# Kernel tuning notes

Measured on AMD Instinct MI355X. Metric: run time of the kernel, lower is better.

## Reference

```python
import jax, jax.numpy as jnp
import numpy as np

NUM_Q = 2048
N = 512
D = 256
H = 8
LW = 25
B = 32
NUM_ATTN = 6  # base, local, skill_group, global, cross_base_local, cross_skill_global


def _layernorm(x, g, b, eps=1e-5):
    m = jnp.mean(x, axis=-1, keepdims=True)
    v = jnp.mean((x - m) ** 2, axis=-1, keepdims=True)
    return (x - m) / jnp.sqrt(v + eps) * g + b


def _mha(q, k, v, in_w, in_b, out_w, out_b, mask=None):
    # torch nn.MultiheadAttention math, batch-first layout. mask: bool, True = masked.
    Bq, Lq, d = q.shape
    Lk = k.shape[1]
    hd = d // H
    qh = (q @ in_w[:d].T + in_b[:d]).reshape(Bq, Lq, H, hd).transpose(0, 2, 1, 3)
    kh = (k @ in_w[d:2 * d].T + in_b[d:2 * d]).reshape(Bq, Lk, H, hd).transpose(0, 2, 1, 3)
    vh = (v @ in_w[2 * d:].T + in_b[2 * d:]).reshape(Bq, Lk, H, hd).transpose(0, 2, 1, 3)
    s = jnp.einsum('bhqd,bhkd->bhqk', qh, kh) / jnp.sqrt(jnp.asarray(hd, q.dtype))
    if mask is not None:
        s = jnp.where(mask, jnp.asarray(-1e9, s.dtype), s)
    w = jax.nn.softmax(s, axis=-1)
    o = jnp.einsum('bhqk,bhkd->bhqd', w, vh).transpose(0, 2, 1, 3).reshape(Bq, Lq, d)
    return o @ out_w.T + out_b, jnp.mean(w, axis=1)  # avg heads like torch default


def setup_inputs() -> dict:
    key = jax.random.key(0)
    ks = jax.random.split(key, 24)
    s = 0.02
    inp = {
        'q': jax.random.randint(ks[0], (B, N), 0, NUM_Q),
        'r': jax.random.randint(ks[1], (B, N), 0, 2),
        'qry': jax.random.randint(ks[2], (B, N), 0, NUM_Q),
        'M_emb': jax.random.normal(ks[3], (NUM_Q * 2, D), jnp.float32) * s,
        'E_emb': jax.random.normal(ks[4], (NUM_Q, D), jnp.float32) * s,
        'P': jax.random.normal(ks[5], (N, D), jnp.float32) * s,
        'attn_in_w': jax.random.normal(ks[6], (NUM_ATTN, 3 * D, D), jnp.float32) * s,
        'attn_in_b': jnp.zeros((NUM_ATTN, 3 * D), jnp.float32),
        'attn_out_w': jax.random.normal(ks[7], (NUM_ATTN, D, D), jnp.float32) * s,
        'attn_out_b': jnp.zeros((NUM_ATTN, D), jnp.float32),
        'skill_cluster_weights': jax.random.normal(ks[8], (NUM_Q, NUM_Q), jnp.float32) * s,
        'skill_proj_w': jax.random.normal(ks[9], (D, NUM_Q), jnp.float32) * s,
        'skill_proj_b': jnp.zeros((D,), jnp.float32),
        'skill_to_embed_w': jax.random.normal(ks[10], (D, N), jnp.float32) * s,
        'skill_to_embed_b': jnp.zeros((D,), jnp.float32),
        'ffn_w1': jax.random.normal(ks[11], (D, D), jnp.float32) * s,
        'ffn_b1': jnp.zeros((D,), jnp.float32),
        'ffn_w2': jax.random.normal(ks[12], (D, D), jnp.float32) * s,
        'ffn_b2': jnp.zeros((D,), jnp.float32),
        'ln1_g': jnp.ones((D,), jnp.float32),
        'ln1_b': jnp.zeros((D,), jnp.float32),
        'ln2_g': jnp.ones((D,), jnp.float32),
        'ln2_b': jnp.zeros((D,), jnp.float32),
        'pred_w': jax.random.normal(ks[13], (1, D), jnp.float32) * s,
        'pred_b': jnp.zeros((1,), jnp.float32),
    }
    return inp


def reference(q, r, qry, M_emb, E_emb, P, attn_in_w, attn_in_b, attn_out_w, attn_out_b,
              skill_cluster_weights, skill_proj_w, skill_proj_b, skill_to_embed_w,
              skill_to_embed_b, ffn_w1, ffn_b1, ffn_w2, ffn_b2, ln1_g, ln1_b, ln2_g,
              ln2_b, pred_w, pred_b):
    bsz = q.shape[0]
    x = q + NUM_Q * r                      # [B, N]
    M = M_emb[x] + P[None]                 # [B, N, D]
    E = E_emb[qry]                         # [B, N, D]
    causal = jnp.triu(jnp.ones((N, N), bool), 1)

    S_base, attn_weights_base = _mha(E, M, M, attn_in_w[0], attn_in_b[0],
                                     attn_out_w[0], attn_out_b[0], causal)
    S_base = _layernorm(S_base + M + E, ln1_g, ln1_b)

    # local windowed causal attention over last LW steps, zeros elsewhere
    loc = S_base[:, -LW:, :]
    local_causal = jnp.triu(jnp.ones((LW, LW), bool), 1)
    S_local, _ = _mha(loc, loc, loc, attn_in_w[1], attn_in_b[1],
                      attn_out_w[1], attn_out_b[1], local_causal)
    S_local = jnp.concatenate(
        [jnp.zeros((bsz, N - LW, D), S_base.dtype), S_local], axis=1)

    # skill-group: one_hot(q) @ softmax(W) == row gather (same math, no dense one-hot)
    sw = jax.nn.softmax(skill_cluster_weights, axis=-1)
    skill_group_repr = sw[q]                                  # [B, N, NUM_Q]
    skill_group_repr = skill_group_repr @ skill_proj_w.T + skill_proj_b  # [B, N, D]
    S_sg = jnp.einsum('bnd,bmd->bnm', S_base, skill_group_repr)          # [B, N, N]
    S_sg = S_sg @ skill_to_embed_w.T + skill_to_embed_b                  # [B, N, D]
    S_sg, _ = _mha(S_sg, S_sg, S_sg, attn_in_w[2], attn_in_b[2],
                   attn_out_w[2], attn_out_b[2])

    S_glob, _ = _mha(S_base, S_base, S_base, attn_in_w[3], attn_in_b[3],
                     attn_out_w[3], attn_out_b[3], causal)

    S_bl, _ = _mha(S_base, S_local, S_local, attn_in_w[4], attn_in_b[4],
                   attn_out_w[4], attn_out_b[4])
    S_sgl, _ = _mha(S_sg, S_glob, S_glob, attn_in_w[5], attn_in_b[5],
                    attn_out_w[5], attn_out_b[5])

    S = S_base + S_local + S_sg + S_glob + S_bl + S_sgl
    F = jax.nn.relu(S @ ffn_w1.T + ffn_b1) @ ffn_w2.T + ffn_b2
    F = _layernorm(F + S, ln2_g, ln2_b)
    p = jax.nn.sigmoid(F @ pred_w.T + pred_b).squeeze(-1)     # [B, N]
    return p, attn_weights_base
```

## Files before the change

### kernel.cpp

```cpp
#include <hip/hip_runtime.h>
#include <hip/hip_bf16.h>

#define B_  32
#define N_  512
#define D_  256
#define H_  8
#define HD_ 32
#define LW_ 25

typedef __hip_bfloat16 bf;
typedef __attribute__((ext_vector_type(8))) short short8;
typedef __attribute__((ext_vector_type(4))) float f32x4;

__device__ __forceinline__ void gload16(const void* g, void* l) {
    __builtin_amdgcn_global_load_lds(
        (const __attribute__((address_space(1))) unsigned int*)g,
        (__attribute__((address_space(3))) unsigned int*)l, 16, 0, 0);
}

#define QSC 0.2550349f

__global__ __launch_bounds__(256) void gemm2_k(
    const bf* Aq, const bf* Akv, const bf* W, const float* bias,
    float* Cf, bf* Cb, float* Cacc,
// ... 29 lines not shown

    const int sidx0 = tid, sidx1 = tid + 256;
    long long arow0, arow1;
    {
        int m = m0 + (sidx0 >> 2);
        arow0 = (long long)(m / rowsPerA) * aBatch + (long long)(m % rowsPerA) * aRstride;
        m = m0 + (sidx1 >> 2);
        arow1 = (long long)(m / rowsPerA) * aBatch + (long long)(m % rowsPerA) * aRstride;
    }
    const long long wrow0 = (long long)(o0 + (sidx0 >> 2)) * K;
    const long long wrow1 = (long long)(o0 + (sidx1 >> 2)) * K;
    const int ac0 = (sidx0 & 3) * 8, ac1 = (sidx1 & 3) * 8;

    f32x4 acc[4][4];
    #pragma unroll
    for (int mt = 0; mt < 4; mt++)
        #pragma unroll
        for (int nt = 0; nt < 4; nt++)
            acc[mt][nt] = (f32x4)0.f;

    for (int k0 = kStart; k0 < kEnd; k0 += 32) {
        const long long ka = (long long)k0 * aKMul;
        gload16(A + arow0 + ka + ac0, As + sidx0 * 8);
        gload16(A + arow1 + ka + ac1, As + sidx1 * 8);
        gload16(Wp + wrow0 + k0 + ac0, Bs + sidx0 * 8);
        gload16(Wp + wrow1 + k0 + ac1, Bs + sidx1 * 8);
        __syncthreads();
        short8 af[4], bfr[4];
        #pragma unroll
        for (int mt = 0; mt < 4; mt++)
            af[mt] = *(const short8*)(As + (wm + mt * 16 + col) * 32 + quad * 8);
        #pragma unroll
        for (int nt = 0; nt < 4; nt++)
            bfr[nt] = *(const short8*)(Bs + (wn + nt * 16 + col) * 32 + quad * 8);
        #pragma unroll
        for (int mt = 0; mt < 4; mt++)
            #pragma unroll
            for (int nt = 0; nt < 4; nt++)
                acc[mt][nt] = __builtin_amdgcn_mfma_f32_16x16x32_bf16(
                    af[mt], bfr[nt], acc[mt][nt], 0, 0, 0);
        __syncthreads();
    }

    #pragma unroll
    for (int mt = 0; mt < 4; mt++) {
        #pragma unroll
        for (int nt = 0; nt < 4; nt++) {
            const int o = o0 + wn + nt * 16 + col;
            #pragma unroll
            for (int r = 0; r < 4; r++) {
                const int m = m0 + wm + mt * 16 + quad * 4 + r;
                if (m >= M) continue;
                float v = acc[mt][nt][r];
                if (bias) v += bias[o];
                if (flags & 1) v = fmaxf(v, 0.f);
                if (flags & 4) {
                    atomicAdd(Cf + (long long)m * Onum + o, v);
                } else {
                    long long ci = (long long)m * Onum + o;
                    if (flags & 2) v += Cf[ci];
                    if (Cf) Cf[ci] = v;
                    if (Cb) Cb[ci] = __float2bfloat16(v);
                    if (Cacc) Cacc[ci] += v;
                }
            }
        }
    }
}

__global__ __launch_bounds__(256) void gemm64_k(
    const bf* A, const bf* W, const float* bias,
    float* Cf, bf* Cb, float* Cacc,
    int M, int K, int Onum,
    int rowsPerA, long long aBatch, int aRstride, long long aKMul,
    long long aZ, long long wZ, long long cZ, int flags)
{
    __shared__ __align__(16) bf As[64 * 32];
    __shared__ __align__(16) bf Bs[64 * 32];
    const int tid = threadIdx.x;
    const int o0 = blockIdx.x * 64;
    const int m0 = blockIdx.y * 64;
    const int z  = blockIdx.z;
    A += (long long)z * aZ;
    W += (long long)z * wZ;
    if (Cf)   Cf   += (long long)z * cZ;
    if (Cb)   Cb   += (long long)z * cZ;
    if (Cacc) Cacc += (long long)z * cZ;

    const int w = tid >> 6, lane = tid & 63;
    const int col = lane & 15, quad = lane >> 4;
    const int wm = (w & 1) * 32;
    const int wn = (w >> 1) * 32;

    const int srow = tid >> 2;
    const int sac  = (tid & 3) * 8;
    long long arow;
    {
        const int m = m0 + srow;
        arow = (long long)(m / rowsPerA) * aBatch
             + (long long)(m % rowsPerA) * aRstride;
    }
    const long long wrow = (long long)(o0 + srow) * K;

    f32x4 acc[2][2];
    acc[0][0] = (f32x4)0.f; acc[0][1] = (f32x4)0.f;
    acc[1][0] = (f32x4)0.f; acc[1][1] = (f32x4)0.f;

    for (int k0 = 0; k0 < K; k0 += 32) {
        gload16(A + arow + (long long)k0 * aKMul + sac, As + tid * 8);
        gload16(W + wrow + k0 + sac, Bs + tid * 8);
        __syncthreads();
        short8 af[2], bfr[2];
        #pragma unroll
        for (int mt = 0; mt < 2; mt++)
            af[mt] = *(const short8*)(As + (wm + mt * 16 + col) * 32 + quad * 8);
        #pragma unroll
        for (int nt = 0; nt < 2; nt++)
            bfr[nt] = *(const short8*)(Bs + (wn + nt * 16 + col) * 32 + quad * 8);
        #pragma unroll
        for (int mt = 0; mt < 2; mt++)
            #pragma unroll
            for (int nt = 0; nt < 2; nt++)
                acc[mt][nt] = __builtin_amdgcn_mfma_f32_16x16x32_bf16(
                    af[mt], bfr[nt], acc[mt][nt], 0, 0, 0);
        __syncthreads();
    }

    #pragma unroll
    for (int mt = 0; mt < 2; mt++) {
        #pragma unroll
        for (int nt = 0; nt < 2; nt++) {
            const int o = o0 + wn + nt * 16 + col;
            #pragma unroll
            for (int r = 0; r < 4; r++) {
                const int m = m0 + wm + mt * 16 + quad * 4 + r;
                if (m >= M) continue;
                float v = acc[mt][nt][r];
                if (bias) v += bias[o];
                if (flags & 1) v = fmaxf(v, 0.f);
                if (flags & 4) {
                    atomicAdd(Cf + (long long)m * Onum + o, v);
                } else {
                    long long ci = (long long)m * Onum + o;
                    if (flags & 2) v += Cf[ci];
                    if (Cf) Cf[ci] = v;
                    if (Cb) Cb[ci] = __float2bfloat16(v);
                    if (Cacc) Cacc[ci] += v;
                }
            }
        }
    }
}

template<int LP2>
__global__ __launch_bounds__(256) void dgemm_k(
    const bf* Aq, const bf* Akv, const bf* W, const float* bias,
    int M, int K,
    int rowsPerA, long long aBatch, int aRstride, long long aKMul,
    bf* Qd, bf* Kd, bf* Vd, int Lseq, int Lvt)
{
    const int tid = threadIdx.x;
    const int w = tid >> 6, lane = tid & 63;
    const int col = lane & 15, quad = lane >> 4;
    const int nmb = gridDim.x / 12;
    int ob, mb;
    if ((nmb & 7) == 0) {
        const int xcd = blockIdx.x & 7;
        const int q = blockIdx.x >> 3;
        mb = xcd + 8 * (q / 12);
        ob = q % 12;
    } else {
        ob = blockIdx.x % 12;
        mb = blockIdx.x / 12;
    }
    const int o0 = ob * 64;
    const int m0 = mb * 128;
    const bf* A = (o0 >= 256) ? Akv : Aq;
    const bf* Wp = W;

    const long long aStep = 32 * aKMul;
    const bf* aP[2];
    #pragma unroll
    for (int mt = 0; mt < 2; mt++) {
        const int m = m0 + w * 32 + mt * 16 + col;
        aP[mt] = A + (long long)(m / rowsPerA) * aBatch
               + (long long)(m % rowsPerA) * aRstride + quad * 8;
    }
    const bf* wP[4];
    #pragma unroll
    for (int ot = 0; ot < 4; ot++)
        wP[ot] = Wp + (long long)(o0 + ot * 16 + col) * K + quad * 8;

    f32x4 acc[2][4];
    #pragma unroll
    for (int mt = 0; mt < 2; mt++)
        #pragma unroll
        for (int ot = 0; ot < 4; ot++)
            acc[mt][ot] = (f32x4)0.f;

    short8 af0 = *(const short8*)aP[0];
    short8 af1 = *(const short8*)aP[1];
    short8 bw[4];
    #pragma unroll
    for (int ot = 0; ot < 4; ot++) bw[ot] = *(const short8*)wP[ot];
    aP[0] += aStep; aP[1] += aStep;
    #pragma unroll
    for (int ot = 0; ot < 4; ot++) wP[ot] += 32;

    const int kc1 = K >> 5;
    for (int kc = 0; kc < kc1 - 1; kc++) {
        short8 naf0 = *(const short8*)aP[0];
        short8 naf1 = *(const short8*)aP[1];
        short8 nbw[4];
        #pragma unroll
        for (int ot = 0; ot < 4; ot++) nbw[ot] = *(const short8*)wP[ot];
        aP[0] += aStep; aP[1] += aStep;
        #pragma unroll
        for (int ot = 0; ot < 4; ot++) wP[ot] += 32;

        #pragma unroll
        for (int ot = 0; ot < 4; ot++) {
            acc[0][ot] = __builtin_amdgcn_mfma_f32_16x16x32_bf16(
                af0, bw[ot], acc[0][ot], 0, 0, 0);
            acc[1][ot] = __builtin_amdgcn_mfma_f32_16x16x32_bf16(
                af1, bw[ot], acc[1][ot], 0, 0, 0);
        }
        af0 = naf0; af1 = naf1;
        #pragma unroll
        for (int ot = 0; ot < 4; ot++) bw[ot] = nbw[ot];
    }
    #pragma unroll
    for (int ot = 0; ot < 4; ot++) {
        acc[0][ot] = __builtin_amdgcn_mfma_f32_16x16x32_bf16(
            af0, bw[ot], acc[0][ot], 0, 0, 0);
        acc[1][ot] = __builtin_amdgcn_mfma_f32_16x16x32_bf16(
            af1, bw[ot], acc[1][ot], 0, 0, 0);
    }

    const int which = o0 >> 8;
    #pragma unroll
    for (int mt = 0; mt < 2; mt++) {
        const int mb4 = m0 + w * 32 + mt * 16 + quad * 4;
        #pragma unroll
        for (int ot = 0; ot < 4; ot++) {
            const int o  = o0 + ot * 16 + col;
            const int j2 = o & 31;
            const int hh = (o >> 5) & 7;
            if (LP2 > 0) {
                const int bb  = mb4 >> LP2;
                const int nn0 = mb4 & ((1 << LP2) - 1);
                const int bh  = bb * H_ + hh;
                float v0 = acc[mt][ot][0], v1 = acc[mt][ot][1],
                      v2 = acc[mt][ot][2], v3 = acc[mt][ot][3];
                if (bias) {
                    const float bv = bias[o];
                    v0 += bv; v1 += bv; v2 += bv; v3 += bv;
                }
                if (which == 0) {
                    bf* q = Qd + ((size_t)bh * Lseq + nn0) * HD_ + j2;
                    q[0]      = __float2bfloat16(v0 * QSC);
                    q[HD_]    = __float2bfloat16(v1 * QSC);
                    q[2*HD_]  = __float2bfloat16(v2 * QSC);
                    q[3*HD_]  = __float2bfloat16(v3 * QSC);
                } else if (which == 1) {
                    bf* kd = Kd + ((size_t)bh * Lseq + nn0) * HD_ + j2;
                    kd[0]     = __float2bfloat16(v0);
                    kd[HD_]   = __float2bfloat16(v1);
                    kd[2*HD_] = __float2bfloat16(v2);
                    kd[3*HD_] = __float2bfloat16(v3);
                } else {
                    __align__(8) bf pk[4];
                    pk[0] = __float2bfloat16(v0);
                    pk[1] = __float2bfloat16(v1);
                    pk[2] = __float2bfloat16(v2);
                    pk[3] = __float2bfloat16(v3);
                    *(ushort4*)(Vd + ((size_t)bh * HD_ + j2) * Lvt + nn0) =
                        *(const ushort4*)pk;
                }
            } else {
                #pragma unroll
                for (int r = 0; r < 4; r++) {
                    const int m = mb4 + r;
                    if (m >= M) continue;
                    float v = acc[mt][ot][r];
                    if (bias) v += bias[o];
                    const int bb = m / Lseq, nn = m % Lseq;
                    const int bh = bb * H_ + hh;
                    if (which == 0) {
                        Qd[((size_t)bh * Lseq + nn) * HD_ + j2] =
                            __float2bfloat16(v * QSC);
                    } else if (which == 1) {
                        Kd[((size_t)bh * Lseq + nn) * HD_ + j2] = __float2bfloat16(v);
                    } else {
                        Vd[((size_t)bh * HD_ + j2) * Lvt + nn] = __float2bfloat16(v);
                    }
                }
            }
        }
    }
}

template<int CAUSAL, int STATS>
__global__ __launch_bounds__(256) void fattn_k(
    const bf* __restrict__ Qb, const bf* __restrict__ Kb,
    const bf* __restrict__ Vtb, bf* __restrict__ O,
    float2* __restrict__ St, int L, int Lvt)
{
    __shared__ __align__(16) bf Sh[4][16][40];
    const int tid = threadIdx.x;
    const int w = tid >> 6, lane = tid & 63;
    const int col = lane & 15, quad = lane >> 4;
    const int bh = blockIdx.x;
    const int yt = CAUSAL ? (int)(gridDim.y - 1 - blockIdx.y) : (int)blockIdx.y;
    const int q0 = yt * 64 + w * 16;
    const int NCH = L >> 5;
    const int cmax = CAUSAL ? min(NCH - 1, (q0 + 15) >> 5) : (NCH - 1);

    const bf* Qh = Qb  + (size_t)bh * L * HD_;
    const bf* Kh = Kb  + (size_t)bh * L * HD_;
    const bf* Vh = Vtb + (size_t)bh * HD_ * Lvt;

    const short8 aq = *(const short8*)(Qh + (size_t)(q0 + col) * HD_ + quad * 8);

    float m[4]   = {-3e38f, -3e38f, -3e38f, -3e38f};
    float sdp[4] = {0.f, 0.f, 0.f, 0.f};
    f32x4 oacc[2];
    oacc[0] = (f32x4)0.f; oacc[1] = (f32x4)0.f;

    const int qrow = q0 + quad * 4;

    auto process = [&](short8 kf0, short8 kf1, short8 vf0, short8 vf1,
                       int c, bool domask) {
        f32x4 s0 = __builtin_amdgcn_mfma_f32_16x16x32_bf16(
            aq, kf0, (f32x4)0.f, 0, 0, 0);
        f32x4 s1 = __builtin_amdgcn_mfma_f32_16x16x32_bf16(
            aq, kf1, (f32x4)0.f, 0, 0, 0);
        if (domask) {
            const int key0 = c * 32 + col;
            #pragma unroll
            for (int r = 0; r < 4; r++) {
                if (key0 > qrow + r)      s0[r] = -1e9f;
                if (key0 + 16 > qrow + r) s1[r] = -1e9f;
            }
        }
        float pml[4];
        #pragma unroll
        for (int r = 0; r < 4; r++)
            pml[r] = fmaxf(s0[r], s1[r]);
        const int okr = (pml[0] <= m[0] + 8.f) && (pml[1] <= m[1] + 8.f)
                     && (pml[2] <= m[2] + 8.f) && (pml[3] <= m[3] + 8.f);
        if (!__all(okr)) {
            #pragma unroll
            for (int r = 0; r < 4; r++) {
                float pm = pml[r];
                #pragma unroll
                for (int off = 1; off < 16; off <<= 1)
                    pm = fmaxf(pm, __shfl_xor(pm, off));
                const float mn = fmaxf(m[r], pm);
                const float scl = __builtin_amdgcn_exp2f(m[r] - mn);
                m[r] = mn;
                sdp[r] *= scl;
                oacc[0][r] *= scl;
                oacc[1][r] *= scl;
            }
        }
        #pragma unroll
        for (int r = 0; r < 4; r++) {
            float e0 = __builtin_amdgcn_exp2f(s0[r] - m[r]);
            float e1 = __builtin_amdgcn_exp2f(s1[r] - m[r]);
            sdp[r] += e0 + e1;
            Sh[w][quad * 4 + r][col]      = __float2bfloat16(e0);
            Sh[w][quad * 4 + r][16 + col] = __float2bfloat16(e1);
        }
        const short8 ap = *(const short8*)(&Sh[w][col][quad * 8]);
        oacc[0] = __builtin_amdgcn_mfma_f32_16x16x32_bf16(ap, vf0, oacc[0], 0, 0, 0);
        oacc[1] = __builtin_amdgcn_mfma_f32_16x16x32_bf16(ap, vf1, oacc[1], 0, 0, 0);
    };

    const bf* kP = Kh + (size_t)col * HD_ + quad * 8;
    const bf* vP = Vh + (size_t)col * Lvt + quad * 8;
    const int kHf = 16 * HD_;
    const int vHf = 16 * Lvt;

    short8 kf0 = *(const short8*)kP;
    short8 kf1 = *(const short8*)(kP + kHf);
    short8 vf0 = *(const short8*)vP;
    short8 vf1 = *(const short8*)(vP + vHf);
    kP += 32 * HD_; vP += 32;

    for (int c = 0; c < cmax; c++) {
        short8 nk0 = *(const short8*)kP;
        short8 nk1 = *(const short8*)(kP + kHf);
        short8 nv0 = *(const short8*)vP;
        short8 nv1 = *(const short8*)(vP + vHf);
        kP += 32 * HD_; vP += 32;
        process(kf0, kf1, vf0, vf1, c, false);
        kf0 = nk0; kf1 = nk1; vf0 = nv0; vf1 = nv1;
    }
    process(kf0, kf1, vf0, vf1, cmax, CAUSAL != 0);

    float inv[4];
    #pragma unroll
    for (int r = 0; r < 4; r++) {
        #pragma unroll
        for (int off = 1; off < 16; off <<= 1)
            sdp[r] += __shfl_xor(sdp[r], off);
        inv[r] = 1.f / sdp[r];
    }
    if (STATS && col == 0) {
        #pragma unroll
        for (int r = 0; r < 4; r++)
            St[(size_t)bh * L + q0 + quad * 4 + r] = make_float2(m[r], inv[r]);
    }
    #pragma unroll
    for (int hf = 0; hf < 2; hf++)
        #pragma unroll
        for (int r = 0; r < 4; r++)
            O[((size_t)bh * L + q0 + quad * 4 + r) * HD_ + hf * 16 + col] =
                __float2bfloat16(oacc[hf][r] * inv[r]);
}

__global__ __launch_bounds__(256) void meanp_k(
    const bf* __restrict__ Qb, const bf* __restrict__ Kb,
    const float2* __restrict__ St, float* __restrict__ meanW)
{
    const int tid = threadIdx.x;
    const int w = tid >> 6, lane = tid & 63;
    const int col = lane & 15, quad = lane >> 4;
    const int b = blockIdx.x;
    const int q0 = blockIdx.y * 16;
    const int cmax = (q0 + 15) >> 5;

    f32x4 mreg[4][2];
    #pragma unroll
    for (int cc = 0; cc < 4; cc++)
        #pragma unroll
        for (int hf = 0; hf < 2; hf++) mreg[cc][hf] = (f32x4)0.f;

    for (int h = 0; h < H_; h++) {
        const int bh = b * H_ + h;
        const bf* Qh = Qb + (size_t)bh * N_ * HD_;
        const bf* Kh = Kb + (size_t)bh * N_ * HD_;
        const short8 aq = *(const short8*)(Qh + (size_t)(q0 + col) * HD_ + quad * 8);
        float mrow[4], irow[4];
        #pragma unroll
        for (int r = 0; r < 4; r++) {
            float2 s2 = St[(size_t)bh * N_ + q0 + quad * 4 + r];
            mrow[r] = s2.x; irow[r] = s2.y;
        }
        #pragma unroll
        for (int cc = 0; cc < 4; cc++) {
            const int c = w + 4 * cc;
            if (c > cmax) continue;
            #pragma unroll
            for (int hf = 0; hf < 2; hf++) {
                const int key = c * 32 + hf * 16 + col;
                const short8 kf = *(const short8*)(Kh + (size_t)key * HD_ + quad * 8);
                f32x4 sc = __builtin_amdgcn_mfma_f32_16x16x32_bf16(
                    aq, kf, (f32x4)0.f, 0, 0, 0);
                #pragma unroll
                for (int r = 0; r < 4; r++) {
                    float p = (key > q0 + quad * 4 + r) ? 0.f
                        : __builtin_amdgcn_exp2f(sc[r] - mrow[r]) * irow[r];
                    mreg[cc][hf][r] += p;
                }
            }
        }
    }

    const size_t base = ((size_t)b * N_ + q0) * N_;
    #pragma unroll
    for (int cc = 0; cc < 4; cc++) {
        const int c = w + 4 * cc;
        #pragma unroll
        for (int hf = 0; hf < 2; hf++)
            #pragma unroll
            for (int r = 0; r < 4; r++)
                meanW[base + (size_t)(quad * 4 + r) * N_ + c * 32 + hf * 16 + col]
                    = mreg[cc][hf][r] * 0.125f;
    }
}

#define SP 520
#define OPS 34

template<int MEAN, int QT>
__global__ __launch_bounds__(256) void attn5_k(
    const bf* Qb, const bf* Kb, const bf* Vtb,
    bf* O, float* meanW, int L, int Lvt, int causal, int nhl)
{
    __shared__ __align__(16) bf Sh[16 * SP];
    __shared__ __align__(16) float redm[2][16][4];
    __shared__ __align__(16) float invRow[16];
    __shared__ __align__(16) float Opart[4][16][OPS];
    const int tid = threadIdx.x;
    const int w = tid >> 6, lane = tid & 63;
    const int col = lane & 15, quad = lane >> 4;
    const int q0 = blockIdx.y * (16 * QT);
    const int bh0 = blockIdx.x * nhl;
    const int NCH = (L + 31) >> 5;
    const int qLast = q0 + (QT - 1) * 16;
    const int cmaxP = causal ? min(NCH - 1, (qLast + 15) >> 5) : (NCH - 1);
    const int nccP = (w <= cmaxP) ? ((cmaxP - w) >> 2) + 1 : 0;

    f32x4 mreg[4][2];
    if (MEAN) {
        #pragma unroll
        for (int cc = 0; cc < 4; cc++)
            #pragma unroll
            for (int hf = 0; hf < 2; hf++) mreg[cc][hf] = (f32x4)0.f;
    }

    for (int hh = 0; hh < nhl; hh++) {
        const int bh = bh0 + hh;
        const bf* Qh = Qb  + (size_t)bh * L * HD_;
        const bf* Kh = Kb  + (size_t)bh * L * HD_;
        const bf* Vh = Vtb + (size_t)bh * HD_ * Lvt;

        short8 aq[QT];
        #pragma unroll
        for (int t = 0; t < QT; t++) {
            aq[t] = (short8)(short)0;
            const int n = q0 + t * 16 + col;
            if (n < L)
                aq[t] = *(const short8*)(Qh + (size_t)n * HD_ + quad * 8);
        }
        short8 kfr[4][2], vfr[4][2];
        #pragma unroll
        for (int cc = 0; cc < 4; cc++) {
            if (cc >= nccP) break;
            const int c = w + 4 * cc;
            #pragma unroll
            for (int hf = 0; hf < 2; hf++) {
                const int key = c * 32 + hf * 16 + col;
                kfr[cc][hf] = (short8)(short)0;
                if (key < L)
                    kfr[cc][hf] = *(const short8*)(Kh + (size_t)key * HD_ + quad * 8);
                vfr[cc][hf] = *(const short8*)(Vh + (size_t)(hf * 16 + col) * Lvt
                                                + c * 32 + quad * 8);
            }
        }

        #pragma unroll
        for (int t = 0; t < QT; t++) {
            const int qt0 = q0 + t * 16;
            const int cmaxT = causal ? min(NCH - 1, (qt0 + 15) >> 5) : (NCH - 1);
            const int nccT = (w <= cmaxT) ? ((cmaxT - w) >> 2) + 1 : 0;

            f32x4 sc[4][2];
            #pragma unroll
            for (int cc = 0; cc < 4; cc++) {
                if (cc >= nccT) break;
// ... 107 lines not shown
            for (int e = tid; e < 512; e += 256) {
                int row = e >> 5, d = e & 31;
                float v = (Opart[0][row][d] + Opart[1][row][d] +
                           Opart[2][row][d] + Opart[3][row][d]) * invRow[row];
                int n = qt0 + row;
                if (n < L)
                    O[((size_t)bh * L + n) * HD_ + d] = __float2bfloat16(v);
            }
            if (t + 1 < QT || hh + 1 < nhl) __syncthreads();
        }
    }

    if (MEAN) {
        const size_t base = ((size_t)blockIdx.x * N_ + q0) * N_;
        #pragma unroll
        for (int cc = 0; cc < 4; cc++) {
            const int c = w + 4 * cc;
            #pragma unroll
            for (int hf = 0; hf < 2; hf++)
                #pragma unroll
                for (int r = 0; r < 4; r++)
                    meanW[base + (size_t)(quad * 4 + r) * N_ + c * 32 + hf * 16 + col]
                        = mreg[cc][hf][r] * 0.125f;
        }
    }
}

__global__ void conv_k(const float* s, bf* d, int n) {
    int i = blockIdx.x * 256 + threadIdx.x;
    if (i < n) d[i] = __float2bfloat16(s[i]);
}

__global__ __launch_bounds__(256) void rowsoftmax_k(const float* in, bf* out) {
    __shared__ float red[256];
    const long long row = blockIdx.x;
    const int t = threadIdx.x;
    const float* ip = in + row * 2048;
    bf* op = out + row * 2048;
    float m = -3e38f;
    for (int k = t; k < 2048; k += 256) m = fmaxf(m, ip[k]);
    red[t] = m; __syncthreads();
    for (int s = 128; s > 0; s >>= 1) { if (t < s) red[t] = fmaxf(red[t], red[t + s]); __syncthreads(); }
    m = red[0]; __syncthreads();
    float ps = 0.f;
    float ev[8];
    #pragma unroll
    for (int i = 0; i < 8; i++) { ev[i] = __expf(ip[t + i * 256] - m); ps += ev[i]; }
    red[t] = ps; __syncthreads();
    for (int s = 128; s > 0; s >>= 1) { if (t < s) red[t] += red[t + s]; __syncthreads(); }
    const float inv = 1.f / red[0];
    #pragma unroll
    for (int i = 0; i < 8; i++) op[t + i * 256] = __float2bfloat16(ev[i] * inv);
}

__global__ void embed_k(const int* q, const int* r, const int* qry,
                        const float* Memb, const float* Eemb, const float* P,
                        float* M, float* E, bf* Mh, bf* Eh) {
    const int i = blockIdx.x; const int t = threadIdx.x;
    const int n = i & (N_ - 1);
    const int x = q[i] + 2048 * r[i];
    float mv = Memb[(long long)x * D_ + t] + P[(long long)n * D_ + t];
    float evv = Eemb[(long long)qry[i] * D_ + t];
    M[(long long)i * D_ + t] = mv;  Mh[(long long)i * D_ + t] = __float2bfloat16(mv);
    E[(long long)i * D_ + t] = evv; Eh[(long long)i * D_ + t] = __float2bfloat16(evv);
}

__global__ void gather_k(const int* q, const float* T, const float* spb, bf* G) {
    const int i = blockIdx.x; const int t = threadIdx.x;
    G[(long long)i * D_ + t] = __float2bfloat16(T[(long long)q[i] * D_ + t] + spb[t]);
}

__global__ __launch_bounds__(256) void ln_k(const float* xa, const float* xb, const float* xc,
                                            const float* g, const float* bta,
                                            float* outF, bf* outB, float* out2) {
    __shared__ float red[256];
    const long long row = blockIdx.x;
    const int t = threadIdx.x;
    float v = xa[row * D_ + t];
    if (xb) v += xb[row * D_ + t];
    if (xc) v += xc[row * D_ + t];
    red[t] = v; __syncthreads();
    for (int s = 128; s > 0; s >>= 1) { if (t < s) red[t] += red[t + s]; __syncthreads(); }
    const float mean = red[0] * (1.f / 256.f);
    __syncthreads();
    const float d = v - mean;
    red[t] = d * d; __syncthreads();
    for (int s = 128; s > 0; s >>= 1) { if (t < s) red[t] += red[t + s]; __syncthreads(); }
    const float var = red[0] * (1.f / 256.f);
    const float y = d * rsqrtf(var + 1e-5f) * g[t] + bta[t];
    if (outF) outF[row * D_ + t] = y;
    if (outB) outB[row * D_ + t] = __float2bfloat16(y);
    if (out2) out2[row * D_ + t] = y;
}

__global__ void scatterlocal_k(const float* tail, bf* Slocalh, float* Sacc) {
    const int i = blockIdx.x; const int t = threadIdx.x;
    const int n = i & (N_ - 1), b = i >> 9;
    float v = 0.f;
    if (n >= N_ - LW_) {
        v = tail[((long long)(b * LW_ + (n - (N_ - LW_)))) * D_ + t];
        Sacc[(long long)i * D_ + t] += v;
    }
    Slocalh[(long long)i * D_ + t] = __float2bfloat16(v);
}

__global__ void zero4_k(float4* p) {
    p[(long long)blockIdx.x * 256 + threadIdx.x] = make_float4(0.f, 0.f, 0.f, 0.f);
}

__global__ __launch_bounds__(256) void pred_k(const float* F, const float* pw, const float* pb,
                                              float* out) {
    const int tid = threadIdx.x;
    const int wave = tid >> 6, lane = tid & 63;
    const long long row = (long long)blockIdx.x * 4 + wave;
    const float* fp = F + row * D_ + lane * 4;
    float s = 0.f;
    #pragma unroll
    for (int j = 0; j < 4; j++) s += fp[j] * pw[lane * 4 + j];
    #pragma unroll
    for (int off = 32; off > 0; off >>= 1) s += __shfl_down(s, off);
    if (lane == 0) {
        float p = 1.f / (1.f + __expf(-(s + pb[0])));
        out[row] = p;
    }
}

static void gemm2(hipStream_t st, const bf* Aq, const bf* Akv,
                  const bf* W, const float* bias, float* Cf, bf* Cb, float* Cacc,
                  int M, int K, int Onum,
                  int rowsPerA, long long aBatch, int aRstride, long long aKMul,
                  long long aZ, long long wZ, long long cZ, int Z,
                  int qkv, int flags, int splitKc,
                  bf* Qd, bf* Kd, bf* Vd, int Lseq, int Lvt)
{
    dim3 g(Onum / 128, (M + 127) / 128, Z), blk(256, 1, 1);
    gemm2_k<<<g, blk, 0, st>>>(Aq, Akv, W, bias, Cf, Cb, Cacc, M, K, Onum,
                               rowsPerA, aBatch, aRstride, aKMul,
                               aZ, wZ, cZ, qkv, flags, splitKc,
                               Qd, Kd, Vd, Lseq, Lvt);
}

static void gemm64(hipStream_t st, const bf* A, const bf* W, const float* bias,
                   float* Cf, bf* Cb, float* Cacc, int M, int K, int Onum,
                   int rowsPerA, long long aBatch, int aRstride, long long aKMul,
                   long long aZ, long long wZ, long long cZ, int Z, int flags)
{
    dim3 g(Onum / 64, (M + 63) / 64, Z), blk(256, 1, 1);
    gemm64_k<<<g, blk, 0, st>>>(A, W, bias, Cf, Cb, Cacc, M, K, Onum,
                                rowsPerA, aBatch, aRstride, aKMul,
                                aZ, wZ, cZ, flags);
}

static void dqkv(hipStream_t st, const bf* Aq, const bf* Akv,
                 const bf* W, const float* bias, int M, int K,
                 int rowsPerA, long long aBatch, int aRstride, long long aKMul,
                 bf* Qd, bf* Kd, bf* Vd, int Lseq, int Lvt)
{
    dim3 g(((M + 127) / 128) * 12, 1, 1), blk(256, 1, 1);
    if (Lseq == 512 && (M & 127) == 0)
        dgemm_k<9><<<g, blk, 0, st>>>(Aq, Akv, W, bias, M, K,
                                      rowsPerA, aBatch, aRstride, aKMul,
                                      Qd, Kd, Vd, Lseq, Lvt);
    else
        dgemm_k<0><<<g, blk, 0, st>>>(Aq, Akv, W, bias, M, K,
                                      rowsPerA, aBatch, aRstride, aKMul,
                                      Qd, Kd, Vd, Lseq, Lvt);
}

extern "C" void kernel_launch(void* const* d_in, const int* in_sizes, int n_in,
                              void* d_out, int out_size, void* d_ws, size_t ws_size,
                              hipStream_t stream)
{
    const int* qi  = (const int*)d_in[0];
    const int* ri  = (const int*)d_in[1];
    const int* qry = (const int*)d_in[2];
    const float* Memb = (const float*)d_in[3];
    const float* Eemb = (const float*)d_in[4];
    const float* Pp   = (const float*)d_in[5];
    const float* ainw = (const float*)d_in[6];
    const float* ainb = (const float*)d_in[7];
    const float* aoutw= (const float*)d_in[8];
    const float* aoutb= (const float*)d_in[9];
    const float* scw  = (const float*)d_in[10];
    const float* spw  = (const float*)d_in[11];
    const float* spb  = (const float*)d_in[12];
    const float* stew = (const float*)d_in[13];
    const float* steb = (const float*)d_in[14];
    const float* fw1  = (const float*)d_in[15];
    const float* fb1  = (const float*)d_in[16];
    const float* fw2  = (const float*)d_in[17];
    const float* fb2  = (const float*)d_in[18];
    const float* l1g  = (const float*)d_in[19];
    const float* l1b  = (const float*)d_in[20];
    const float* l2g  = (const float*)d_in[21];
    const float* l2b  = (const float*)d_in[22];
    const float* pw   = (const float*)d_in[23];
    const float* pb   = (const float*)d_in[24];
    float* out = (float*)d_out;
    float* outW = out + B_ * N_;

    const size_t BND = (size_t)B_ * N_ * D_;
    float* ws = (float*)d_ws;
    float* b10 = ws;
    float* b0  = ws + 1 * BND;
    float* b1  = ws + 2 * BND;
    float* b8  = ws + 3 * BND;
    float* b9  = ws + 4 * BND;
    float* hp  = ws + 5 * BND;
    bf* b0h  = (bf*)(hp + 0 * (BND / 2));
    bf* b1h  = (bf*)(hp + 1 * (BND / 2));
    bf* b2h  = (bf*)(hp + 2 * (BND / 2));
    bf* b7h  = (bf*)(hp + 3 * (BND / 2));
    bf* b8h  = (bf*)(hp + 4 * (BND / 2));
    bf* b9h  = (bf*)(hp + 5 * (BND / 2));
    bf* b10h = (bf*)(hp + 6 * (BND / 2));
    bf* b11h = (bf*)(hp + 7 * (BND / 2));
    bf* Qb   = (bf*)(hp + 8 * (BND / 2));
    bf* Kb   = (bf*)(hp + 9 * (BND / 2));
    bf* Vtb  = (bf*)(hp + 10 * (BND / 2));
    bf* Ob   = (bf*)(hp + 11 * (BND / 2));
    bf* BNNb = (bf*)(hp + 12 * (BND / 2));
    float* Ttab = hp + 12 * (BND / 2) + BND;
    bf* SWb  = (bf*)(Ttab + 2048 * 256);
    bf* Wb   = SWb + (size_t)2048 * 2048;
    bf* ainwB = Wb;
    bf* aoutwB = ainwB + 6 * 768 * 256;
    bf* spwB  = aoutwB + 6 * 256 * 256;
    bf* stewB = spwB + 256 * 2048;
    bf* fw1B  = stewB + 256 * 512;
    bf* fw2B  = fw1B + 256 * 256;
    const int BNrows = B_ * N_;
    const int BH = B_ * H_;
    const long long OBAT = 8LL * N_ * HD_;
    const long long OBATL = 8LL * LW_ * HD_;

    conv_k<<<(6*768*256 + 255)/256, 256, 0, stream>>>(ainw, ainwB, 6*768*256);
    conv_k<<<(6*256*256 + 255)/256, 256, 0, stream>>>(aoutw, aoutwB, 6*256*256);
    conv_k<<<(256*2048 + 255)/256, 256, 0, stream>>>(spw, spwB, 256*2048);
    conv_k<<<(256*512 + 255)/256, 256, 0, stream>>>(stew, stewB, 256*512);
    conv_k<<<(256*256 + 255)/256, 256, 0, stream>>>(fw1, fw1B, 256*256);
    conv_k<<<(256*256 + 255)/256, 256, 0, stream>>>(fw2, fw2B, 256*256);

    rowsoftmax_k<<<2048, 256, 0, stream>>>(scw, SWb);
    zero4_k<<<(2048 * 256) / 1024, 256, 0, stream>>>((float4*)Ttab);
    gemm2(stream, SWb, SWb, spwB, nullptr, Ttab, nullptr, nullptr, 2048, 2048, 256,
          2048, 0, 2048, 1, 0, 0, 0, 8, 0, 4, 256, nullptr, nullptr, nullptr, 0, 0);

    embed_k<<<BNrows, 256, 0, stream>>>(qi, ri, qry, Memb, Eemb, Pp, b0, b1, b0h, b1h);

    dqkv(stream, b1h, b0h, ainwB + 0, ainb + 0, BNrows, 256,
         BNrows, 0, 256, 1, Qb, Kb, Vtb, N_, N_);
    fattn_k<1, 1><<<dim3(BH, 8), 256, 0, stream>>>(Qb, Kb, Vtb, Ob, (float2*)b8, N_, N_);
    meanp_k<<<dim3(B_, 32), 256, 0, stream>>>(Qb, Kb, (const float2*)b8, outW);
    gemm64(stream, Ob, aoutwB + 0, aoutb + 0, b10, nullptr, nullptr, BNrows, 256, 256,
           N_, OBAT, HD_, N_, 0, 0, 0, 1, 0);
    ln_k<<<BNrows, 256, 0, stream>>>(b10, b0, b1, l1g, l1b, nullptr, b2h, b10);

    dqkv(stream, b2h + (size_t)(N_ - LW_) * D_, b2h + (size_t)(N_ - LW_) * D_,
         ainwB + 1 * 196608, ainb + 768, B_ * LW_, 256,
         LW_, (long long)N_ * D_, 256, 1, Qb, Kb, Vtb, LW_, 32);
    attn5_k<0, 2><<<dim3(BH, 1), 256, 0, stream>>>(Qb, Kb, Vtb, Ob, nullptr, LW_, 32, 1, 1);
    gemm64(stream, Ob, aoutwB + 1 * 65536, aoutb + 256, b0, nullptr, nullptr, B_ * LW_,
           256, 256, LW_, OBATL, HD_, LW_, 0, 0, 0, 1, 0);
    scatterlocal_k<<<BNrows, 256, 0, stream>>>(b0, b7h, b10);

    gather_k<<<BNrows, 256, 0, stream>>>(qi, Ttab, spb, b1h);
    gemm64(stream, b2h, b1h, nullptr, nullptr, BNNb, nullptr, N_, 256, N_,
           N_, 0, 256, 1, (long long)N_ * D_, (long long)N_ * D_, (long long)N_ * N_,
           B_, 0);
    gemm64(stream, BNNb, stewB, steb, nullptr, b11h, nullptr, BNrows, 512, 256,
           BNrows, 0, 512, 1, 0, 0, 0, 1, 0);
    dqkv(stream, b11h, b11h, ainwB + 2 * 196608, ainb + 2 * 768, BNrows, 256,
         BNrows, 0, 256, 1, Qb, Kb, Vtb, N_, N_);
    fattn_k<0, 0><<<dim3(BH, 8), 256, 0, stream>>>(Qb, Kb, Vtb, Ob, nullptr, N_, N_);
    gemm64(stream, Ob, aoutwB + 2 * 65536, aoutb + 2 * 256, b8, b8h, b10, BNrows,
           256, 256, N_, OBAT, HD_, N_, 0, 0, 0, 1, 0);

    dqkv(stream, b2h, b2h, ainwB + 3 * 196608, ainb + 3 * 768, BNrows, 256,
         BNrows, 0, 256, 1, Qb, Kb, Vtb, N_, N_);
    fattn_k<1, 0><<<dim3(BH, 8), 256, 0, stream>>>(Qb, Kb, Vtb, Ob, nullptr, N_, N_);
    gemm64(stream, Ob, aoutwB + 3 * 65536, aoutb + 3 * 256, b9, b9h, b10, BNrows,
           256, 256, N_, OBAT, HD_, N_, 0, 0, 0, 1, 0);

    dqkv(stream, b2h, b7h, ainwB + 4 * 196608, ainb + 4 * 768, BNrows, 256,
         BNrows, 0, 256, 1, Qb, Kb, Vtb, N_, N_);
    fattn_k<0, 0><<<dim3(BH, 8), 256, 0, stream>>>(Qb, Kb, Vtb, Ob, nullptr, N_, N_);
    gemm64(stream, Ob, aoutwB + 4 * 65536, aoutb + 4 * 256, b10, nullptr, nullptr, BNrows,
           256, 256, N_, OBAT, HD_, N_, 0, 0, 0, 1, 2);

    dqkv(stream, b8h, b9h, ainwB + 5 * 196608, ainb + 5 * 768, BNrows, 256,
         BNrows, 0, 256, 1, Qb, Kb, Vtb, N_, N_);
    fattn_k<0, 0><<<dim3(BH, 8), 256, 0, stream>>>(Qb, Kb, Vtb, Ob, nullptr, N_, N_);
    gemm64(stream, Ob, aoutwB + 5 * 65536, aoutb + 5 * 256, b10, b10h, nullptr, BNrows,
           256, 256, N_, OBAT, HD_, N_, 0, 0, 0, 1, 2);

    gemm64(stream, b10h, fw1B, fb1, nullptr, b11h, nullptr, BNrows, 256, 256,
           BNrows, 0, 256, 1, 0, 0, 0, 1, 1);
    gemm64(stream, b11h, fw2B, fb2, b0, nullptr, nullptr, BNrows, 256, 256,
           BNrows, 0, 256, 1, 0, 0, 0, 1, 0);
    ln_k<<<BNrows, 256, 0, stream>>>(b0, b10, nullptr, l2g, l2b, b1, nullptr, nullptr);
    pred_k<<<BNrows / 4, 256, 0, stream>>>(b1, pw, pb, out);
}
```

Measured before the change: 850.4 us.

## Software-pipeline flash attention PV with double-buffered P; fully unroll QKV GEMM K loop

The attention kernel now computes the P·V MFMA for the previous key chunk while the current chunk's QK scores and softmax are computed, using a double-buffered shared-memory P tile and a peeled first and last iteration. The first chunk initialises the running max directly instead of starting from a sentinel. The QKV projection GEMM makes K a template constant and fully unrolls the K loop, replacing the manual register prefetch. This hides MFMA and LDS latency at the cost of more registers and more complex control flow, which could reduce occupancy.

```diff
diff --git a/kernel.cpp b/kernel.cpp
--- a/kernel.cpp
+++ b/kernel.cpp
@@ -205,10 +205,10 @@
     }
 }
 
-template<int LP2>
+template<int LP2, int KC>
 __global__ __launch_bounds__(256) void dgemm_k(
     const bf* Aq, const bf* Akv, const bf* W, const float* bias,
-    int M, int K,
+    int M,
     int rowsPerA, long long aBatch, int aRstride, long long aKMul,
     bf* Qd, bf* Kd, bf* Vd, int Lseq, int Lvt)
 {
@@ -229,9 +229,8 @@
     const int o0 = ob * 64;
     const int m0 = mb * 128;
     const bf* A = (o0 >= 256) ? Akv : Aq;
-    const bf* Wp = W;
-
-    const long long aStep = 32 * aKMul;
+    const int K = KC * 32;
+
     const bf* aP[2];
     #pragma unroll
     for (int mt = 0; mt < 2; mt++) {
@@ -242,7 +241,7 @@
     const bf* wP[4];
     #pragma unroll
     for (int ot = 0; ot < 4; ot++)
-        wP[ot] = Wp + (long long)(o0 + ot * 16 + col) * K + quad * 8;
+        wP[ot] = W + (long long)(o0 + ot * 16 + col) * K + quad * 8;
 
     f32x4 acc[2][4];
     #pragma unroll
@@ -251,43 +250,19 @@
         for (int ot = 0; ot < 4; ot++)
             acc[mt][ot] = (f32x4)0.f;
 
-    short8 af0 = *(const short8*)aP[0];
-    short8 af1 = *(const short8*)aP[1];
-    short8 bw[4];
-    #pragma unroll
-    for (int ot = 0; ot < 4; ot++) bw[ot] = *(const short8*)wP[ot];
-    aP[0] += aStep; aP[1] += aStep;
-    #pragma unroll
-    for (int ot = 0; ot < 4; ot++) wP[ot] += 32;
-
-    const int kc1 = K >> 5;
-    for (int kc = 0; kc < kc1 - 1; kc++) {
-        short8 naf0 = *(const short8*)aP[0];
-        short8 naf1 = *(const short8*)aP[1];
-        short8 nbw[4];
-        #pragma unroll
-        for (int ot = 0; ot < 4; ot++) nbw[ot] = *(const short8*)wP[ot];
-        aP[0] += aStep; aP[1] += aStep;
-        #pragma unroll
-        for (int ot = 0; ot < 4; ot++) wP[ot] += 32;
-
+    #pragma unroll
+    for (int kc = 0; kc < KC; kc++) {
+        const long long ka = (long long)kc * 32 * aKMul;
+        const short8 af0 = *(const short8*)(aP[0] + ka);
+        const short8 af1 = *(const short8*)(aP[1] + ka);
         #pragma unroll
         for (int ot = 0; ot < 4; ot++) {
+            const short8 bfg = *(const short8*)(wP[ot] + kc * 32);
             acc[0][ot] = __builtin_amdgcn_mfma_f32_16x16x32_bf16(
-                af0, bw[ot], acc[0][ot], 0, 0, 0);
+                af0, bfg, acc[0][ot], 0, 0, 0);
             acc[1][ot] = __builtin_amdgcn_mfma_f32_16x16x32_bf16(
-                af1, bw[ot], acc[1][ot], 0, 0, 0);
-        }
-        af0 = naf0; af1 = naf1;
-        #pragma unroll
-        for (int ot = 0; ot < 4; ot++) bw[ot] = nbw[ot];
-    }
-    #pragma unroll
-    for (int ot = 0; ot < 4; ot++) {
-        acc[0][ot] = __builtin_amdgcn_mfma_f32_16x16x32_bf16(
-            af0, bw[ot], acc[0][ot], 0, 0, 0);
-        acc[1][ot] = __builtin_amdgcn_mfma_f32_16x16x32_bf16(
-            af1, bw[ot], acc[1][ot], 0, 0, 0);
+                af1, bfg, acc[1][ot], 0, 0, 0);
+        }
     }
 
     const int which = o0 >> 8;
@@ -359,7 +334,7 @@
     const bf* __restrict__ Vtb, bf* __restrict__ O,
     float2* __restrict__ St, int L, int Lvt)
 {
-    __shared__ __align__(16) bf Sh[4][16][40];
+    __shared__ __align__(16) bf Sh[4][2][16][40];
     const int tid = threadIdx.x;
     const int w = tid >> 6, lane = tid & 63;
     const int col = lane & 15, quad = lane >> 4;
@@ -375,27 +350,77 @@
 
     const short8 aq = *(const short8*)(Qh + (size_t)(q0 + col) * HD_ + quad * 8);
 
-    float m[4]   = {-3e38f, -3e38f, -3e38f, -3e38f};
+    float m[4];
     float sdp[4] = {0.f, 0.f, 0.f, 0.f};
     f32x4 oacc[2];
     oacc[0] = (f32x4)0.f; oacc[1] = (f32x4)0.f;
 
     const int qrow = q0 + quad * 4;
-
-    auto process = [&](short8 kf0, short8 kf1, short8 vf0, short8 vf1,
-                       int c, bool domask) {
+    const int kHf = 16 * HD_;
+    const int vHf = 16 * Lvt;
+
+    const bf* kP = Kh + (size_t)col * HD_ + quad * 8;
+    const bf* vP = Vh + (size_t)col * Lvt + quad * 8;
+
+    short8 kf0 = *(const short8*)kP;
+    short8 kf1 = *(const short8*)(kP + kHf);
+    short8 vp0 = *(const short8*)vP;
+    short8 vp1 = *(const short8*)(vP + vHf);
+    kP += 32 * HD_; vP += 32;
+    short8 kn0 = *(const short8*)kP;
+    short8 kn1 = *(const short8*)(kP + kHf);
+    short8 vn0 = *(const short8*)vP;
+    short8 vn1 = *(const short8*)(vP + vHf);
+    kP += 32 * HD_; vP += 32;
+
+    {
         f32x4 s0 = __builtin_amdgcn_mfma_f32_16x16x32_bf16(
             aq, kf0, (f32x4)0.f, 0, 0, 0);
         f32x4 s1 = __builtin_amdgcn_mfma_f32_16x16x32_bf16(
             aq, kf1, (f32x4)0.f, 0, 0, 0);
-        if (domask) {
-            const int key0 = c * 32 + col;
+        if (CAUSAL && cmax == 0) {
+            const int key0 = col;
             #pragma unroll
             for (int r = 0; r < 4; r++) {
                 if (key0 > qrow + r)      s0[r] = -1e9f;
                 if (key0 + 16 > qrow + r) s1[r] = -1e9f;
             }
         }
+        #pragma unroll
+        for (int r = 0; r < 4; r++) {
+            float pm = fmaxf(s0[r], s1[r]);
+            #pragma unroll
+            for (int off = 1; off < 16; off <<= 1)
+                pm = fmaxf(pm, __shfl_xor(pm, off));
+            m[r] = pm;
+            float e0 = __builtin_amdgcn_exp2f(s0[r] - pm);
+            float e1 = __builtin_amdgcn_exp2f(s1[r] - pm);
+            sdp[r] = e0 + e1;
+            Sh[w][0][quad * 4 + r][col]      = __float2bfloat16(e0);
+            Sh[w][0][quad * 4 + r][16 + col] = __float2bfloat16(e1);
+        }
+    }
+    kf0 = kn0; kf1 = kn1;
+    short8 vc0 = vn0, vc1 = vn1;
+
+    for (int c = 1; c < cmax; c++) {
+        kn0 = *(const short8*)kP;
+        kn1 = *(const short8*)(kP + kHf);
+        vn0 = *(const short8*)vP;
+        vn1 = *(const short8*)(vP + vHf);
+        kP += 32 * HD_; vP += 32;
+
+        f32x4 s0 = __builtin_amdgcn_mfma_f32_16x16x32_bf16(
+            aq, kf0, (f32x4)0.f, 0, 0, 0);
+        f32x4 s1 = __builtin_amdgcn_mfma_f32_16x16x32_bf16(
+            aq, kf1, (f32x4)0.f, 0, 0, 0);
+
+        {
+            const short8 ap = *(const short8*)(&Sh[w][(c - 1) & 1][col][quad * 8]);
+            oacc[0] = __builtin_amdgcn_mfma_f32_16x16x32_bf16(ap, vp0, oacc[0], 0, 0, 0);
+            oacc[1] = __builtin_amdgcn_mfma_f32_16x16x32_bf16(ap, vp1, oacc[1], 0, 0, 0);
+        }
+
         float pml[4];
         #pragma unroll
         for (int r = 0; r < 4; r++)
@@ -417,40 +442,76 @@
                 oacc[1][r] *= scl;
             }
         }
+
         #pragma unroll
         for (int r = 0; r < 4; r++) {
             float e0 = __builtin_amdgcn_exp2f(s0[r] - m[r]);
             float e1 = __builtin_amdgcn_exp2f(s1[r] - m[r]);
             sdp[r] += e0 + e1;
-            Sh[w][quad * 4 + r][col]      = __float2bfloat16(e0);
-            Sh[w][quad * 4 + r][16 + col] = __float2bfloat16(e1);
-        }
-        const short8 ap = *(const short8*)(&Sh[w][col][quad * 8]);
-        oacc[0] = __builtin_amdgcn_mfma_f32_16x16x32_bf16(ap, vf0, oacc[0], 0, 0, 0);
-        oacc[1] = __builtin_amdgcn_mfma_f32_16x16x32_bf16(ap, vf1, oacc[1], 0, 0, 0);
-    };
-
-    const bf* kP = Kh + (size_t)col * HD_ + quad * 8;
-    const bf* vP = Vh + (size_t)col * Lvt + quad * 8;
-    const int kHf = 16 * HD_;
-    const int vHf = 16 * Lvt;
-
-    short8 kf0 = *(const short8*)kP;
-    short8 kf1 = *(const short8*)(kP + kHf);
-    short8 vf0 = *(const short8*)vP;
-    short8 vf1 = *(const short8*)(vP + vHf);
-    kP += 32 * HD_; vP += 32;
-
-    for (int c = 0; c < cmax; c++) {
-        short8 nk0 = *(const short8*)kP;
-        short8 nk1 = *(const short8*)(kP + kHf);
-        short8 nv0 = *(const short8*)vP;
-        short8 nv1 = *(const short8*)(vP + vHf);
-        kP += 32 * HD_; vP += 32;
-        process(kf0, kf1, vf0, vf1, c, false);
-        kf0 = nk0; kf1 = nk1; vf0 = nv0; vf1 = nv1;
-    }
-    process(kf0, kf1, vf0, vf1, cmax, CAUSAL != 0);
+            Sh[w][c & 1][quad * 4 + r][col]      = __float2bfloat16(e0);
+            Sh[w][c & 1][quad * 4 + r][16 + col] = __float2bfloat16(e1);
+        }
+
+        vp0 = vc0; vp1 = vc1;
+        vc0 = vn0; vc1 = vn1;
+        kf0 = kn0; kf1 = kn1;
+    }
+
+    if (cmax >= 1) {
+        f32x4 s0 = __builtin_amdgcn_mfma_f32_16x16x32_bf16(
+            aq, kf0, (f32x4)0.f, 0, 0, 0);
+        f32x4 s1 = __builtin_amdgcn_mfma_f32_16x16x32_bf16(
+            aq, kf1, (f32x4)0.f, 0, 0, 0);
+        if (CAUSAL) {
+            const int key0 = cmax * 32 + col;
+            #pragma unroll
+            for (int r = 0; r < 4; r++) {
+                if (key0 > qrow + r)      s0[r] = -1e9f;
+                if (key0 + 16 > qrow + r) s1[r] = -1e9f;
+            }
+        }
+        {
+            const short8 ap = *(const short8*)(&Sh[w][(cmax - 1) & 1][col][quad * 8]);
+            oacc[0] = __builtin_amdgcn_mfma_f32_16x16x32_bf16(ap, vp0, oacc[0], 0, 0, 0);
+            oacc[1] = __builtin_amdgcn_mfma_f32_16x16x32_bf16(ap, vp1, oacc[1], 0, 0, 0);
+        }
+        float pml[4];
+        #pragma unroll
+        for (int r = 0; r < 4; r++)
+            pml[r] = fmaxf(s0[r], s1[r]);
+        const int okr = (pml[0] <= m[0] + 8.f) && (pml[1] <= m[1] + 8.f)
+                     && (pml[2] <= m[2] + 8.f) && (pml[3] <= m[3] + 8.f);
+        if (!__all(okr)) {
+            #pragma unroll
+            for (int r = 0; r < 4; r++) {
+                float pm = pml[r];
+                #pragma unroll
+                for (int off = 1; off < 16; off <<= 1)
+                    pm = fmaxf(pm, __shfl_xor(pm, off));
+                const float mn = fmaxf(m[r], pm);
+                const float scl = __builtin_amdgcn_exp2f(m[r] - mn);
+                m[r] = mn;
+                sdp[r] *= scl;
+                oacc[0][r] *= scl;
+                oacc[1][r] *= scl;
+            }
+        }
+        #pragma unroll
+        for (int r = 0; r < 4; r++) {
+            float e0 = __builtin_amdgcn_exp2f(s0[r] - m[r]);
+            float e1 = __builtin_amdgcn_exp2f(s1[r] - m[r]);
+            sdp[r] += e0 + e1;
+            Sh[w][cmax & 1][quad * 4 + r][col]      = __float2bfloat16(e0);
+            Sh[w][cmax & 1][quad * 4 + r][16 + col] = __float2bfloat16(e1);
+        }
+        vp0 = vc0; vp1 = vc1;
+    }
+
+    {
+        const short8 ap = *(const short8*)(&Sh[w][cmax & 1][col][quad * 8]);
+        oacc[0] = __builtin_amdgcn_mfma_f32_16x16x32_bf16(ap, vp0, oacc[0], 0, 0, 0);
+        oacc[1] = __builtin_amdgcn_mfma_f32_16x16x32_bf16(ap, vp1, oacc[1], 0, 0, 0);
+    }
 
     float inv[4];
     #pragma unroll
@@ -864,19 +925,19 @@
 }
 
 static void dqkv(hipStream_t st, const bf* Aq, const bf* Akv,
-                 const bf* W, const float* bias, int M, int K,
+                 const bf* W, const float* bias, int M,
                  int rowsPerA, long long aBatch, int aRstride, long long aKMul,
                  bf* Qd, bf* Kd, bf* Vd, int Lseq, int Lvt)
 {
     dim3 g(((M + 127) / 128) * 12, 1, 1), blk(256, 1, 1);
     if (Lseq == 512 && (M & 127) == 0)
-        dgemm_k<9><<<g, blk, 0, st>>>(Aq, Akv, W, bias, M, K,
-                                      rowsPerA, aBatch, aRstride, aKMul,
-                                      Qd, Kd, Vd, Lseq, Lvt);
+        dgemm_k<9, 8><<<g, blk, 0, st>>>(Aq, Akv, W, bias, M,
+                                         rowsPerA, aBatch, aRstride, aKMul,
+                                         Qd, Kd, Vd, Lseq, Lvt);
     else
-        dgemm_k<0><<<g, blk, 0, st>>>(Aq, Akv, W, bias, M, K,
-                                      rowsPerA, aBatch, aRstride, aKMul,
-                                      Qd, Kd, Vd, Lseq, Lvt);
+        dgemm_k<0, 8><<<g, blk, 0, st>>>(Aq, Akv, W, bias, M,
+                                         rowsPerA, aBatch, aRstride, aKMul,
+                                         Qd, Kd, Vd, Lseq, Lvt);
 }
 
 extern "C" void kernel_launch(void* const* d_in, const int* in_sizes, int n_in,
@@ -960,7 +1021,7 @@
 
     embed_k<<<BNrows, 256, 0, stream>>>(qi, ri, qry, Memb, Eemb, Pp, b0, b1, b0h, b1h);
 
-    dqkv(stream, b1h, b0h, ainwB + 0, ainb + 0, BNrows, 256,
+    dqkv(stream, b1h, b0h, ainwB + 0, ainb + 0, BNrows,
          BNrows, 0, 256, 1, Qb, Kb, Vtb, N_, N_);
     fattn_k<1, 1><<<dim3(BH, 8), 256, 0, stream>>>(Qb, Kb, Vtb, Ob, (float2*)b8, N_, N_);
     meanp_k<<<dim3(B_, 32), 256, 0, stream>>>(Qb, Kb, (const float2*)b8, outW);
@@ -969,7 +1030,7 @@
     ln_k<<<BNrows, 256, 0, stream>>>(b10, b0, b1, l1g, l1b, nullptr, b2h, b10);
 
     dqkv(stream, b2h + (size_t)(N_ - LW_) * D_, b2h + (size_t)(N_ - LW_) * D_,
-         ainwB + 1 * 196608, ainb + 768, B_ * LW_, 256,
+         ainwB + 1 * 196608, ainb + 768, B_ * LW_,
          LW_, (long long)N_ * D_, 256, 1, Qb, Kb, Vtb, LW_, 32);
     attn5_k<0, 2><<<dim3(BH, 1), 256, 0, stream>>>(Qb, Kb, Vtb, Ob, nullptr, LW_, 32, 1, 1);
     gemm64(stream, Ob, aoutwB + 1 * 65536, aoutb + 256, b0, nullptr, nullptr, B_ * LW_,
@@ -982,25 +1043,25 @@
            B_, 0);
     gemm64(stream, BNNb, stewB, steb, nullptr, b11h, nullptr, BNrows, 512, 256,
            BNrows, 0, 512, 1, 0, 0, 0, 1, 0);
-    dqkv(stream, b11h, b11h, ainwB + 2 * 196608, ainb + 2 * 768, BNrows, 256,
+    dqkv(stream, b11h, b11h, ainwB + 2 * 196608, ainb + 2 * 768, BNrows,
          BNrows, 0, 256, 1, Qb, Kb, Vtb, N_, N_);
     fattn_k<0, 0><<<dim3(BH, 8), 256, 0, stream>>>(Qb, Kb, Vtb, Ob, nullptr, N_, N_);
     gemm64(stream, Ob, aoutwB + 2 * 65536, aoutb + 2 * 256, b8, b8h, b10, BNrows,
            256, 256, N_, OBAT, HD_, N_, 0, 0, 0, 1, 0);
 
-    dqkv(stream, b2h, b2h, ainwB + 3 * 196608, ainb + 3 * 768, BNrows, 256,
+    dqkv(stream, b2h, b2h, ainwB + 3 * 196608, ainb + 3 * 768, BNrows,
          BNrows, 0, 256, 1, Qb, Kb, Vtb, N_, N_);
     fattn_k<1, 0><<<dim3(BH, 8), 256, 0, stream>>>(Qb, Kb, Vtb, Ob, nullptr, N_, N_);
     gemm64(stream, Ob, aoutwB + 3 * 65536, aoutb + 3 * 256, b9, b9h, b10, BNrows,
            256, 256, N_, OBAT, HD_, N_, 0, 0, 0, 1, 0);
 
-    dqkv(stream, b2h, b7h, ainwB + 4 * 196608, ainb + 4 * 768, BNrows, 256,
+    dqkv(stream, b2h, b7h, ainwB + 4 * 196608, ainb + 4 * 768, BNrows,
          BNrows, 0, 256, 1, Qb, Kb, Vtb, N_, N_);
     fattn_k<0, 0><<<dim3(BH, 8), 256, 0, stream>>>(Qb, Kb, Vtb, Ob, nullptr, N_, N_);
     gemm64(stream, Ob, aoutwB + 4 * 65536, aoutb + 4 * 256, b10, nullptr, nullptr, BNrows,
            256, 256, N_, OBAT, HD_, N_, 0, 0, 0, 1, 2);
 
-    dqkv(stream, b8h, b9h, ainwB + 5 * 196608, ainb + 5 * 768, BNrows, 256,
+    dqkv(stream, b8h, b9h, ainwB + 5 * 196608, ainb + 5 * 768, BNrows,
          BNrows, 0, 256, 1, Qb, Kb, Vtb, N_, N_);
     fattn_k<0, 0><<<dim3(BH, 8), 256, 0, stream>>>(Qb, Kb, Vtb, Ob, nullptr, N_, N_);
     gemm64(stream, Ob, aoutwB + 5 * 65536, aoutb + 5 * 256, b10, b10h, nullptr, BNrows,
```

Result: slower. 891.1 us (+4.8%).
